# Kernel optimization log

Hardware: AMD Instinct MI355X
Metric: run time of the kernel (lower is better)

The kernel has to match this reference:

```python
import jax, jax.numpy as jnp
import numpy as np

EMBED = 1024
HEADS = 16
HEAD_DIM = EMBED // HEADS


def setup_inputs() -> dict:
    key = jax.random.key(0)
    ks = jax.random.split(key, 8)
    N, L = 2, 2048
    values = jax.random.normal(ks[0], (N, L, EMBED), dtype=jnp.float32)
    keys_ = jax.random.normal(ks[1], (N, L, EMBED), dtype=jnp.float32)
    query = jax.random.normal(ks[2], (N, L, EMBED), dtype=jnp.float32)
    mask = jnp.ones((N, 1, 1, L), dtype=jnp.int32)
    s = 1.0 / np.sqrt(EMBED)
    W_q = jax.random.normal(ks[3], (EMBED, EMBED), dtype=jnp.float32) * s
    W_k = jax.random.normal(ks[4], (EMBED, EMBED), dtype=jnp.float32) * s
    W_v = jax.random.normal(ks[5], (EMBED, EMBED), dtype=jnp.float32) * s
    W_o = jax.random.normal(ks[6], (EMBED, EMBED), dtype=jnp.float32) * s
    b_o = jax.random.normal(ks[7], (EMBED,), dtype=jnp.float32) * 0.01
    return {"values": values, "keys": keys_, "query": query, "mask": mask,
            "W_q": W_q, "W_k": W_k, "W_v": W_v, "W_o": W_o, "b_o": b_o}


def reference(values, keys, query, mask, W_q, W_k, W_v, W_o, b_o):
    N, Lq, _ = query.shape
    Lk = keys.shape[1]
    # projections (torch Linear: x @ W.T); reshape to (N, H, L, Dh)
    q = (query @ W_q.T).reshape(N, Lq, HEADS, HEAD_DIM).transpose(0, 2, 1, 3)
    k = (keys @ W_k.T).reshape(N, Lk, HEADS, HEAD_DIM).transpose(0, 2, 1, 3)
    v = (values @ W_v.T).reshape(N, Lk, HEADS, HEAD_DIM).transpose(0, 2, 1, 3)
    energy = jnp.einsum('bhqd,bhkd->bhqk', q, k) / jnp.sqrt(jnp.float32(HEAD_DIM))
    energy = jnp.where(mask == 0, jnp.float32(-1e20), energy)
    attn = jax.nn.softmax(energy, axis=-1)
    out = jnp.einsum('bhqk,bhkd->bhqd', attn, v)
    out = out.transpose(0, 2, 1, 3).reshape(N, Lq, EMBED)
    return out @ W_o.T + b_o
```

## Files before the change

### kernel.cpp

```cpp
#include <hip/hip_runtime.h>
#include <cstddef>
#include <cstdint>

#define SEQ    2048
#define NBATCH 2

typedef unsigned short u16;
typedef unsigned int   u32;
typedef __attribute__((ext_vector_type(8))) short bf16x8;
typedef __attribute__((ext_vector_type(4))) float f32x4;

#if __has_builtin(__builtin_amdgcn_exp2f)
#define EXP2F(x) __builtin_amdgcn_exp2f(x)
#else
#define EXP2F(x) exp2f(x)
#endif

__device__ __forceinline__ u32 fbits(float x) { union { float f; u32 u; } c; c.f = x; return c.u; }
__device__ __forceinline__ u16 f2bf(float x) { return (u16)((fbits(x) + 0x8000u) >> 16); }
__device__ __forceinline__ u32 pack2bf(float lo, float hi) {
    return __builtin_amdgcn_perm(fbits(hi) + 0x8000u, fbits(lo) + 0x8000u, 0x07060302u);
}

__global__ __launch_bounds__(256)
void cast3(const float* __restrict__ a, const float* __restrict__ b, const float* __restrict__ c,
           u16* __restrict__ oa, u16* __restrict__ ob, u16* __restrict__ oc, int n4)
{
    const float* s; u16* d;
    if (blockIdx.y == 0)      { s = a; d = oa; }
    else if (blockIdx.y == 1) { s = b; d = ob; }
    else                      { s = c; d = oc; }
    int i = blockIdx.x * 256 + threadIdx.x;
    if (i >= n4) return;
    float4 v = ((const float4*)s)[i];
    uint2 r; r.x = pack2bf(v.x, v.y); r.y = pack2bf(v.z, v.w);
    ((uint2*)d)[i] = r;
}

__global__ __launch_bounds__(256)
void cast4(const float* __restrict__ a, const float* __restrict__ b,
           const float* __restrict__ c, const float* __restrict__ e,
           u16* __restrict__ oa, u16* __restrict__ ob, u16* __restrict__ oc, u16* __restrict__ oe,
           int n4)
{
    const float* s; u16* d;
    if (blockIdx.y == 0)      { s = a; d = oa; }
    else if (blockIdx.y == 1) { s = b; d = ob; }
    else if (blockIdx.y == 2) { s = c; d = oc; }
    else                      { s = e; d = oe; }
    int i = blockIdx.x * 256 + threadIdx.x;
    if (i >= n4) return;
    float4 v = ((const float4*)s)[i];
    uint2 r; r.x = pack2bf(v.x, v.y); r.y = pack2bf(v.z, v.w);
    ((uint2*)d)[i] = r;
}

__device__ __forceinline__
void gemm_body(const u16* __restrict__ X, const u16* __restrict__ W,
               void* __restrict__ Yv, const float* __restrict__ bias, const int layout,
               const int kbeg, const int kend)
{
    __shared__ u16 smem[2 * 128 * 72];
    u16* As = smem;
    u16* Bs = smem + 128 * 72;

    const int tid  = threadIdx.x;
    const int wave = tid >> 6;
    const int lane = tid & 63;
    const int lm   = lane & 15;
    const int quad = lane >> 4;
    const int m0 = blockIdx.x * 128;
    const int n0 = blockIdx.y * 128;
    const int wr = (wave & 1) * 64;
    const int wc = (wave >> 1) * 64;

    const int srow = tid >> 1;
    const int scol = (tid & 1) * 32;
    const u16* xg = X + (size_t)(m0 + srow) * 1024 + scol;
    const u16* wg = W + (size_t)(n0 + srow) * 1024 + scol;

    bf16x8 pa[4], pb[4];
    #pragma unroll
    for (int p = 0; p < 4; ++p) {
        pa[p] = *(const bf16x8*)(xg + kbeg + p * 8);
        pb[p] = *(const bf16x8*)(wg + kbeg + p * 8);
    }

    f32x4 acc[4][4] = {};

    for (int k0 = kbeg; k0 < kend; k0 += 64) {
        __syncthreads();
        #pragma unroll
        for (int p = 0; p < 4; ++p) {
            *(bf16x8*)&As[srow * 72 + scol + p * 8] = pa[p];
            *(bf16x8*)&Bs[srow * 72 + scol + p * 8] = pb[p];
        }
        __syncthreads();
        if (k0 + 64 < kend) {
            #pragma unroll
            for (int p = 0; p < 4; ++p) {
                pa[p] = *(const bf16x8*)(xg + k0 + 64 + p * 8);
                pb[p] = *(const bf16x8*)(wg + k0 + 64 + p * 8);
            }
        }
        #pragma unroll
        for (int kk = 0; kk < 64; kk += 32) {
            bf16x8 af[4], bf[4];
            #pragma unroll
            for (int t = 0; t < 4; ++t) {
                af[t] = *(const bf16x8*)&As[(wr + t * 16 + lm) * 72 + kk + quad * 8];
                bf[t] = *(const bf16x8*)&Bs[(wc + t * 16 + lm) * 72 + kk + quad * 8];
            }
            #pragma unroll
            for (int i = 0; i < 4; ++i)
                #pragma unroll
                for (int j = 0; j < 4; ++j)
                    acc[i][j] = __builtin_amdgcn_mfma_f32_16x16x32_bf16(af[i], bf[j], acc[i][j], 0, 0, 0);
        }
    }

    if (layout == 3) {
        float* Y = (float*)Yv;
        #pragma unroll
        for (int i = 0; i < 4; ++i)
            #pragma unroll
            for (int j = 0; j < 4; ++j) {
                const int C = n0 + wc + j * 16 + lm;
                const float bv = bias ? bias[C] : 0.0f;
                #pragma unroll
                for (int r = 0; r < 4; ++r) {
                    const int R = m0 + wr + i * 16 + quad * 4 + r;
                    Y[(size_t)R * 1024 + C] = acc[i][j][r] + bv;
                }
            }
    } else if (layout == 0) {
        u16* Y = (u16*)Yv;
        #pragma unroll
        for (int i = 0; i < 4; ++i)
            #pragma unroll
            for (int j = 0; j < 4; ++j) {
                const int C = n0 + wc + j * 16 + lm;
                #pragma unroll
                for (int r = 0; r < 4; ++r) {
                    const int R = m0 + wr + i * 16 + quad * 4 + r;
                    Y[(size_t)R * 1024 + C] = f2bf(acc[i][j][r]);
                }
            }
    } else {
        __syncthreads();
        u16* T = smem;
        #pragma unroll
        for (int i = 0; i < 4; ++i)
            #pragma unroll
            for (int j = 0; j < 4; ++j) {
                const int col = wc + j * 16 + lm;
                const int row = wr + i * 16 + quad * 4;
                uint2 v;
                v.x = pack2bf(acc[i][j][0], acc[i][j][1]);
                v.y = pack2bf(acc[i][j][2], acc[i][j][3]);
                *(uint2*)&T[col * 132 + row] = v;
            }
        __syncthreads();
        const int dp = tid >> 1, half = (tid & 1) * 64;
        const int nn = m0 >> 11, l0 = m0 & 2047;
        const int C = n0 + dp, h = C >> 6, d = C & 63;
        u16* Y = (u16*)Yv;
        const size_t base = (((size_t)nn * 16 + h) * 64 + d) * SEQ + l0 + half;
        #pragma unroll
        for (int p = 0; p < 8; ++p) {
            bf16x8 v = *(const bf16x8*)&T[dp * 132 + half + p * 8];
            *(bf16x8*)(Y + base + p * 8) = v;
        }
    }
}

__global__ __launch_bounds__(256, 2)
void gemm_qkv(const u16* __restrict__ xq, const u16* __restrict__ xk, const u16* __restrict__ xv,
              const u16* __restrict__ wq, const u16* __restrict__ wk, const u16* __restrict__ wv,
              u16* __restrict__ qb, u16* __restrict__ kb, u16* __restrict__ vt)
{
    if (blockIdx.z == 0)      gemm_body(xq, wq, qb, nullptr, 0, 0, 1024);
    else if (blockIdx.z == 1) gemm_body(xk, wk, kb, nullptr, 0, 0, 1024);
    else                      gemm_body(xv, wv, vt, nullptr, 2, 0, 1024);
}

__global__ __launch_bounds__(256, 2)
void gemm_out_split(const u16* __restrict__ X, const u16* __restrict__ W,
                    float* __restrict__ p0, float* __restrict__ p1)
{
    if (blockIdx.z == 0) gemm_body(X, W, p0, nullptr, 3, 0, 512);
    else                 gemm_body(X, W, p1, nullptr, 3, 512, 1024);
}

__global__ __launch_bounds__(256)
void reduce_bias(const float* __restrict__ p0, const float* __restrict__ p1,
                 const float* __restrict__ bias, float* __restrict__ out)
{
    const int i = blockIdx.x * 256 + threadIdx.x;
    float4 a = ((const float4*)p0)[i];
    float4 b = ((const float4*)p1)[i];
    float4 c = ((const float4*)bias)[i & 255];
    float4 o;
    o.x = a.x + b.x + c.x; o.y = a.y + b.y + c.y;
    o.z = a.z + b.z + c.z; o.w = a.w + b.w + c.w;
    ((float4*)out)[i] = o;
}

__global__ __launch_bounds__(256, 2)
void flash_attn_bf16(const u16* __restrict__ Qb, const u16* __restrict__ Kb,
                     const u16* __restrict__ VT, const int* __restrict__ mask,
                     u16* __restrict__ O)
{
    __shared__ u16 Ks[128 * 72];
    __shared__ u16 Vts[64 * 136];
    __shared__ u16 Ps[4][32 * 72];

    const int tid  = threadIdx.x;
    const int wave = tid >> 6;
    const int lane = tid & 63;
    const int lm   = lane & 15;
    const int quad = lane >> 4;
    const int h = blockIdx.y, n = blockIdx.z;
    const int wq = blockIdx.x * 128 + wave * 32;

    const u16* Qh = Qb + ((size_t)n * SEQ) * 1024 + h * 64;
    const u16* Kh = Kb + ((size_t)n * SEQ) * 1024 + h * 64;
    const u16* Vh = VT + (((size_t)n * 16 + h) * 64) * SEQ;
    const int* mk = mask + (size_t)n * SEQ;
    u16* Pw = &Ps[wave][0];

    bf16x8 qf[2][2];
    #pragma unroll
    for (int t = 0; t < 2; ++t)
        #pragma unroll
        for (int s = 0; s < 2; ++s)
            qf[t][s] = *(const bf16x8*)(Qh + (size_t)(wq + t * 16 + lm) * 1024 + s * 32 + quad * 8);

    f32x4 o_acc[2][4] = {};
    float l_i[2][4] = {};

    const int kr = tid >> 1, kc = (tid & 1) * 32;
    const int vr = tid >> 2, vc = (tid & 3) * 32;

    bf16x8 ka[4], va[4];
    #pragma unroll
    for (int p = 0; p < 4; ++p) {
        ka[p] = *(const bf16x8*)(Kh + (size_t)kr * 1024 + kc + p * 8);
        va[p] = *(const bf16x8*)(Vh + (size_t)vr * SEQ + vc + p * 8);
    }

    const float cs = 0.125f * 1.44269504f;

    for (int c0 = 0; c0 < SEQ; c0 += 128) {
        __syncthreads();
        #pragma unroll
        for (int p = 0; p < 4; ++p) {
            *(bf16x8*)&Ks[kr * 72 + kc + p * 8]   = ka[p];
            *(bf16x8*)&Vts[vr * 136 + vc + p * 8] = va[p];
        }
        __syncthreads();

        if (c0 + 128 < SEQ) {
            #pragma unroll
            for (int p = 0; p < 4; ++p) {
                ka[p] = *(const bf16x8*)(Kh + (size_t)(c0 + 128 + kr) * 1024 + kc + p * 8);
                va[p] = *(const bf16x8*)(Vh + (size_t)vr * SEQ + c0 + 128 + vc + p * 8);
            }
        }

        f32x4 s[2][8] = {};
        #pragma unroll
        for (int nt = 0; nt < 8; ++nt) {
            bf16x8 kf0 = *(const bf16x8*)&Ks[(nt * 16 + lm) * 72 + quad * 8];
            bf16x8 kf1 = *(const bf16x8*)&Ks[(nt * 16 + lm) * 72 + 32 + quad * 8];
            #pragma unroll
            for (int t = 0; t < 2; ++t) {
                s[t][nt] = __builtin_amdgcn_mfma_f32_16x16x32_bf16(qf[t][0], kf0, s[t][nt], 0, 0, 0);
                s[t][nt] = __builtin_amdgcn_mfma_f32_16x16x32_bf16(qf[t][1], kf1, s[t][nt], 0, 0, 0);
            }
        }

        int msk[8];
        #pragma unroll
        for (int nt = 0; nt < 8; ++nt) msk[nt] = mk[c0 + nt * 16 + lm];
        #pragma unroll
        for (int t = 0; t < 2; ++t)
            #pragma unroll
            for (int nt = 0; nt < 8; ++nt)
                #pragma unroll
                for (int r = 0; r < 4; ++r) {
                    float e = EXP2F(s[t][nt][r] * cs);
                    e = msk[nt] ? e : 0.0f;
                    s[t][nt][r] = e;
                    l_i[t][r] += e;
                }

        #pragma unroll
        for (int half = 0; half < 2; ++half) {
            #pragma unroll
            for (int t = 0; t < 2; ++t)
                #pragma unroll
                for (int ntl = 0; ntl < 4; ++ntl)
                    #pragma unroll
                    for (int r = 0; r < 4; ++r)
                        Pw[(t * 16 + quad * 4 + r) * 72 + ntl * 16 + lm] =
                            f2bf(s[t][half * 4 + ntl][r]);

            #pragma unroll
            for (int ksl = 0; ksl < 2; ++ksl) {
                bf16x8 pf[2];
                #pragma unroll
                for (int t = 0; t < 2; ++t)
                    pf[t] = *(const bf16x8*)&Pw[(t * 16 + lm) * 72 + ksl * 32 + quad * 8];
                #pragma unroll
                for (int dt = 0; dt < 4; ++dt) {
                    bf16x8 vf = *(const bf16x8*)&Vts[(dt * 16 + lm) * 136 + half * 64 + ksl * 32 + quad * 8];
                    #pragma unroll
                    for (int t = 0; t < 2; ++t)
                        o_acc[t][dt] = __builtin_amdgcn_mfma_f32_16x16x32_bf16(pf[t], vf, o_acc[t][dt], 0, 0, 0);
                }
            }
        }
    }

    #pragma unroll
    for (int t = 0; t < 2; ++t)
        #pragma unroll
        for (int r = 0; r < 4; ++r) {
            float v = l_i[t][r];
            #pragma unroll
            for (int off = 1; off < 16; off <<= 1) v += __shfl_xor(v, off);
            l_i[t][r] = 1.0f / v;
        }
    #pragma unroll
    for (int t = 0; t < 2; ++t)
        #pragma unroll
        for (int dt = 0; dt < 4; ++dt)
            #pragma unroll
            for (int r = 0; r < 4; ++r) {
                const int ql = wq + t * 16 + quad * 4 + r;
                const int col = h * 64 + dt * 16 + lm;
                O[((size_t)n * SEQ + ql) * 1024 + col] = f2bf(o_acc[t][dt][r] * l_i[t][r]);
            }
}

extern "C" void kernel_launch(void* const* d_in, const int* in_sizes, int n_in,
                              void* d_out, int out_size, void* d_ws, size_t ws_size,
                              hipStream_t stream)
{
    const float* values = (const float*)d_in[0];
    const float* keys   = (const float*)d_in[1];
    const float* query  = (const float*)d_in[2];
    const int*   mask   = (const int*)d_in[3];
    const float* W_q    = (const float*)d_in[4];
    const float* W_k    = (const float*)d_in[5];
    const float* W_v    = (const float*)d_in[6];
    const float* W_o    = (const float*)d_in[7];
    const float* b_o    = (const float*)d_in[8];

    const size_t NTOK = (size_t)NBATCH * SEQ * 1024;
    const size_t WSZ  = 1024 * 1024;
    u16* p = (u16*)d_ws;
    u16* qb    = p; p += NTOK;
    u16* kb    = p; p += NTOK;
    u16* vt    = p; p += NTOK;
    u16* xq    = p; p += NTOK;
    u16* xk    = p; p += NTOK;
    u16* xv    = p; p += NTOK;
    u16* attnb = p; p += NTOK;
    u16* wqb   = p; p += WSZ;
    u16* wkb   = p; p += WSZ;
    u16* wvb   = p; p += WSZ;
    u16* wob   = p; p += WSZ;
    float* part0 = (float*)qb;
    float* part1 = (float*)vt;

    cast3<<<dim3(4096, 3), 256, 0, stream>>>(query, keys, values, xq, xk, xv, (int)(NTOK / 4));
    cast4<<<dim3(1024, 4), 256, 0, stream>>>(W_q, W_k, W_v, W_o, wqb, wkb, wvb, wob, (int)(WSZ / 4));

    gemm_qkv<<<dim3(32, 8, 3), 256, 0, stream>>>(xq, xk, xv, wqb, wkb, wvb, qb, kb, vt);

    flash_attn_bf16<<<dim3(16, 16, 2), 256, 0, stream>>>(qb, kb, vt, mask, attnb);

    gemm_out_split<<<dim3(32, 8, 2), 256, 0, stream>>>(attnb, wob, part0, part1);
    reduce_bias<<<4096, 256, 0, stream>>>(part0, part1, b_o, (float*)d_out);
}
```

Before: 236.9 us.

## Keep attention probabilities in registers and replace split-K output GEMM with 64-wide tiles

The attention kernel now computes S transposed (K as the A operand) so that each lane's exp values map directly onto the operand layout of the 16x16x16 bf16 MFMA. This removes the per-wave LDS staging buffer for P and its store and reload round-trip, and it also removes that LDS allocation. Row sums are reduced with fewer shuffles, and the mask is loaded as int4 vectors. The output projection drops split-K plus the separate reduce kernel and uses a 128x64 tile with the bias fused into the epilogue. This avoids the fp32 partial buffer round-trip and one launch, at the cost of a smaller-K MFMA instruction in the PV product.

```diff
diff --git a/kernel.cpp b/kernel.cpp
--- a/kernel.cpp
+++ b/kernel.cpp
@@ -8,6 +8,7 @@
 typedef unsigned short u16;
 typedef unsigned int   u32;
 typedef __attribute__((ext_vector_type(8))) short bf16x8;
+typedef __attribute__((ext_vector_type(4))) short bf16x4;
 typedef __attribute__((ext_vector_type(4))) float f32x4;
 
 #if __has_builtin(__builtin_amdgcn_exp2f)
@@ -16,10 +17,15 @@
 #define EXP2F(x) exp2f(x)
 #endif
 
+#define MFMA_K16(a, b, c) __builtin_amdgcn_mfma_f32_16x16x16bf16_1k(a, b, c, 0, 0, 0)
+
 __device__ __forceinline__ u32 fbits(float x) { union { float f; u32 u; } c; c.f = x; return c.u; }
 __device__ __forceinline__ u16 f2bf(float x) { return (u16)((fbits(x) + 0x8000u) >> 16); }
 __device__ __forceinline__ u32 pack2bf(float lo, float hi) {
     return __builtin_amdgcn_perm(fbits(hi) + 0x8000u, fbits(lo) + 0x8000u, 0x07060302u);
+}
+__device__ __forceinline__ bf16x4 mk_bf16x4(u32 lo, u32 hi) {
+    union { u32 w[2]; bf16x4 v; } u; u.w[0] = lo; u.w[1] = hi; return u.v;
 }
 
 __global__ __launch_bounds__(256)
@@ -57,8 +63,7 @@
 
 __device__ __forceinline__
 void gemm_body(const u16* __restrict__ X, const u16* __restrict__ W,
-               void* __restrict__ Yv, const float* __restrict__ bias, const int layout,
-               const int kbeg, const int kend)
+               void* __restrict__ Yv, const int layout)
 {
     __shared__ u16 smem[2 * 128 * 72];
     u16* As = smem;
@@ -82,13 +87,13 @@
     bf16x8 pa[4], pb[4];
     #pragma unroll
     for (int p = 0; p < 4; ++p) {
-        pa[p] = *(const bf16x8*)(xg + kbeg + p * 8);
-        pb[p] = *(const bf16x8*)(wg + kbeg + p * 8);
+        pa[p] = *(const bf16x8*)(xg + p * 8);
+        pb[p] = *(const bf16x8*)(wg + p * 8);
     }
 
     f32x4 acc[4][4] = {};
 
-    for (int k0 = kbeg; k0 < kend; k0 += 64) {
+    for (int k0 = 0; k0 < 1024; k0 += 64) {
         __syncthreads();
         #pragma unroll
         for (int p = 0; p < 4; ++p) {
@@ -96,7 +101,7 @@
             *(bf16x8*)&Bs[srow * 72 + scol + p * 8] = pb[p];
         }
         __syncthreads();
-        if (k0 + 64 < kend) {
+        if (k0 + 64 < 1024) {
             #pragma unroll
             for (int p = 0; p < 4; ++p) {
                 pa[p] = *(const bf16x8*)(xg + k0 + 64 + p * 8);
@@ -119,21 +124,7 @@
         }
     }
 
-    if (layout == 3) {
-        float* Y = (float*)Yv;
-        #pragma unroll
-        for (int i = 0; i < 4; ++i)
-            #pragma unroll
-            for (int j = 0; j < 4; ++j) {
-                const int C = n0 + wc + j * 16 + lm;
-                const float bv = bias ? bias[C] : 0.0f;
-                #pragma unroll
-                for (int r = 0; r < 4; ++r) {
-                    const int R = m0 + wr + i * 16 + quad * 4 + r;
-                    Y[(size_t)R * 1024 + C] = acc[i][j][r] + bv;
-                }
-            }
-    } else if (layout == 0) {
+    if (layout == 0) {
         u16* Y = (u16*)Yv;
         #pragma unroll
         for (int i = 0; i < 4; ++i)
@@ -179,31 +170,83 @@
               const u16* __restrict__ wq, const u16* __restrict__ wk, const u16* __restrict__ wv,
               u16* __restrict__ qb, u16* __restrict__ kb, u16* __restrict__ vt)
 {
-    if (blockIdx.z == 0)      gemm_body(xq, wq, qb, nullptr, 0, 0, 1024);
-    else if (blockIdx.z == 1) gemm_body(xk, wk, kb, nullptr, 0, 0, 1024);
-    else                      gemm_body(xv, wv, vt, nullptr, 2, 0, 1024);
+    if (blockIdx.z == 0)      gemm_body(xq, wq, qb, 0);
+    else if (blockIdx.z == 1) gemm_body(xk, wk, kb, 0);
+    else                      gemm_body(xv, wv, vt, 2);
 }
 
 __global__ __launch_bounds__(256, 2)
-void gemm_out_split(const u16* __restrict__ X, const u16* __restrict__ W,
-                    float* __restrict__ p0, float* __restrict__ p1)
-{
-    if (blockIdx.z == 0) gemm_body(X, W, p0, nullptr, 3, 0, 512);
-    else                 gemm_body(X, W, p1, nullptr, 3, 512, 1024);
-}
-
-__global__ __launch_bounds__(256)
-void reduce_bias(const float* __restrict__ p0, const float* __restrict__ p1,
-                 const float* __restrict__ bias, float* __restrict__ out)
-{
-    const int i = blockIdx.x * 256 + threadIdx.x;
-    float4 a = ((const float4*)p0)[i];
-    float4 b = ((const float4*)p1)[i];
-    float4 c = ((const float4*)bias)[i & 255];
-    float4 o;
-    o.x = a.x + b.x + c.x; o.y = a.y + b.y + c.y;
-    o.z = a.z + b.z + c.z; o.w = a.w + b.w + c.w;
-    ((float4*)out)[i] = o;
+void gemm_out64(const u16* __restrict__ X, const u16* __restrict__ W,
+                float* __restrict__ Y, const float* __restrict__ bias)
+{
+    __shared__ u16 As[128 * 72];
+    __shared__ u16 Bs[64 * 72];
+
+    const int tid  = threadIdx.x;
+    const int wave = tid >> 6;
+    const int lane = tid & 63;
+    const int lm   = lane & 15;
+    const int quad = lane >> 4;
+    const int m0 = blockIdx.x * 128;
+    const int n0 = blockIdx.y * 64;
+    const int wr = (wave & 1) * 64;
+    const int wc = (wave >> 1) * 32;
+
+    const int arow = tid >> 1, acol = (tid & 1) * 32;
+    const int brow = tid >> 2, bcol = (tid & 3) * 16;
+    const u16* xg = X + (size_t)(m0 + arow) * 1024 + acol;
+    const u16* wg = W + (size_t)(n0 + brow) * 1024 + bcol;
+
+    bf16x8 pa[4], pb[2];
+    #pragma unroll
+    for (int p = 0; p < 4; ++p) pa[p] = *(const bf16x8*)(xg + p * 8);
+    #pragma unroll
+    for (int p = 0; p < 2; ++p) pb[p] = *(const bf16x8*)(wg + p * 8);
+
+    f32x4 acc[4][2] = {};
+
+    for (int k0 = 0; k0 < 1024; k0 += 64) {
+        __syncthreads();
+        #pragma unroll
+        for (int p = 0; p < 4; ++p) *(bf16x8*)&As[arow * 72 + acol + p * 8] = pa[p];
+        #pragma unroll
+        for (int p = 0; p < 2; ++p) *(bf16x8*)&Bs[brow * 72 + bcol + p * 8] = pb[p];
+        __syncthreads();
+        if (k0 + 64 < 1024) {
+            #pragma unroll
+            for (int p = 0; p < 4; ++p) pa[p] = *(const bf16x8*)(xg + k0 + 64 + p * 8);
+            #pragma unroll
+            for (int p = 0; p < 2; ++p) pb[p] = *(const bf16x8*)(wg + k0 + 64 + p * 8);
+        }
+        #pragma unroll
+        for (int kk = 0; kk < 64; kk += 32) {
+            bf16x8 af[4], bf[2];
+            #pragma unroll
+            for (int t = 0; t < 4; ++t)
+                af[t] = *(const bf16x8*)&As[(wr + t * 16 + lm) * 72 + kk + quad * 8];
+            #pragma unroll
+            for (int j = 0; j < 2; ++j)
+                bf[j] = *(const bf16x8*)&Bs[(wc + j * 16 + lm) * 72 + kk + quad * 8];
+            #pragma unroll
+            for (int i = 0; i < 4; ++i)
+                #pragma unroll
+                for (int j = 0; j < 2; ++j)
+                    acc[i][j] = __builtin_amdgcn_mfma_f32_16x16x32_bf16(af[i], bf[j], acc[i][j], 0, 0, 0);
+        }
+    }
+
+    #pragma unroll
+    for (int i = 0; i < 4; ++i)
+        #pragma unroll
+        for (int j = 0; j < 2; ++j) {
+            const int C = n0 + wc + j * 16 + lm;
+            const float bv = bias[C];
+            #pragma unroll
+            for (int r = 0; r < 4; ++r) {
+                const int R = m0 + wr + i * 16 + quad * 4 + r;
+                Y[(size_t)R * 1024 + C] = acc[i][j][r] + bv;
+            }
+        }
 }
 
 __global__ __launch_bounds__(256, 2)
@@ -213,7 +256,6 @@
 {
     __shared__ u16 Ks[128 * 72];
     __shared__ u16 Vts[64 * 136];
-    __shared__ u16 Ps[4][32 * 72];
 
     const int tid  = threadIdx.x;
     const int wave = tid >> 6;
@@ -227,17 +269,16 @@
     const u16* Kh = Kb + ((size_t)n * SEQ) * 1024 + h * 64;
     const u16* Vh = VT + (((size_t)n * 16 + h) * 64) * SEQ;
     const int* mk = mask + (size_t)n * SEQ;
-    u16* Pw = &Ps[wave][0];
 
     bf16x8 qf[2][2];
     #pragma unroll
-    for (int t = 0; t < 2; ++t)
-        #pragma unroll
-        for (int s = 0; s < 2; ++s)
-            qf[t][s] = *(const bf16x8*)(Qh + (size_t)(wq + t * 16 + lm) * 1024 + s * 32 + quad * 8);
+    for (int qt = 0; qt < 2; ++qt)
+        #pragma unroll
+        for (int ks = 0; ks < 2; ++ks)
+            qf[qt][ks] = *(const bf16x8*)(Qh + (size_t)(wq + qt * 16 + lm) * 1024 + ks * 32 + quad * 8);
 
     f32x4 o_acc[2][4] = {};
-    float l_i[2][4] = {};
+    float l_i[2] = {};
 
     const int kr = tid >> 1, kc = (tid & 1) * 32;
     const int vr = tid >> 2, vc = (tid & 3) * 32;
@@ -268,79 +309,72 @@
             }
         }
 
-        f32x4 s[2][8] = {};
-        #pragma unroll
-        for (int nt = 0; nt < 8; ++nt) {
-            bf16x8 kf0 = *(const bf16x8*)&Ks[(nt * 16 + lm) * 72 + quad * 8];
-            bf16x8 kf1 = *(const bf16x8*)&Ks[(nt * 16 + lm) * 72 + 32 + quad * 8];
-            #pragma unroll
-            for (int t = 0; t < 2; ++t) {
-                s[t][nt] = __builtin_amdgcn_mfma_f32_16x16x32_bf16(qf[t][0], kf0, s[t][nt], 0, 0, 0);
-                s[t][nt] = __builtin_amdgcn_mfma_f32_16x16x32_bf16(qf[t][1], kf1, s[t][nt], 0, 0, 0);
-            }
-        }
-
-        int msk[8];
-        #pragma unroll
-        for (int nt = 0; nt < 8; ++nt) msk[nt] = mk[c0 + nt * 16 + lm];
-        #pragma unroll
-        for (int t = 0; t < 2; ++t)
-            #pragma unroll
-            for (int nt = 0; nt < 8; ++nt)
+        int4 mkv[8];
+        #pragma unroll
+        for (int kt = 0; kt < 8; ++kt)
+            mkv[kt] = *(const int4*)(mk + c0 + kt * 16 + quad * 4);
+
+        f32x4 st[8][2] = {};
+        #pragma unroll
+        for (int kt = 0; kt < 8; ++kt) {
+            bf16x8 kf0 = *(const bf16x8*)&Ks[(kt * 16 + lm) * 72 + quad * 8];
+            bf16x8 kf1 = *(const bf16x8*)&Ks[(kt * 16 + lm) * 72 + 32 + quad * 8];
+            #pragma unroll
+            for (int qt = 0; qt < 2; ++qt) {
+                st[kt][qt] = __builtin_amdgcn_mfma_f32_16x16x32_bf16(kf0, qf[qt][0], st[kt][qt], 0, 0, 0);
+                st[kt][qt] = __builtin_amdgcn_mfma_f32_16x16x32_bf16(kf1, qf[qt][1], st[kt][qt], 0, 0, 0);
+            }
+        }
+
+        bf16x4 pf[8][2];
+        #pragma unroll
+        for (int kt = 0; kt < 8; ++kt) {
+            const int4 mv = mkv[kt];
+            const int mm[4] = {mv.x, mv.y, mv.z, mv.w};
+            #pragma unroll
+            for (int qt = 0; qt < 2; ++qt) {
+                float e[4];
                 #pragma unroll
                 for (int r = 0; r < 4; ++r) {
-                    float e = EXP2F(s[t][nt][r] * cs);
-                    e = msk[nt] ? e : 0.0f;
-                    s[t][nt][r] = e;
-                    l_i[t][r] += e;
+                    float v = EXP2F(st[kt][qt][r] * cs);
+                    v = mm[r] ? v : 0.0f;
+                    e[r] = v;
+                    l_i[qt] += v;
                 }
-
-        #pragma unroll
-        for (int half = 0; half < 2; ++half) {
-            #pragma unroll
-            for (int t = 0; t < 2; ++t)
+                pf[kt][qt] = mk_bf16x4(pack2bf(e[0], e[1]), pack2bf(e[2], e[3]));
+            }
+        }
+
+        #pragma unroll
+        for (int kt = 0; kt < 8; ++kt)
+            #pragma unroll
+            for (int dt = 0; dt < 4; ++dt) {
+                bf16x4 vf = *(const bf16x4*)&Vts[(dt * 16 + lm) * 136 + kt * 16 + quad * 4];
                 #pragma unroll
-                for (int ntl = 0; ntl < 4; ++ntl)
-                    #pragma unroll
-                    for (int r = 0; r < 4; ++r)
-                        Pw[(t * 16 + quad * 4 + r) * 72 + ntl * 16 + lm] =
-                            f2bf(s[t][half * 4 + ntl][r]);
-
-            #pragma unroll
-            for (int ksl = 0; ksl < 2; ++ksl) {
-                bf16x8 pf[2];
-                #pragma unroll
-                for (int t = 0; t < 2; ++t)
-                    pf[t] = *(const bf16x8*)&Pw[(t * 16 + lm) * 72 + ksl * 32 + quad * 8];
-                #pragma unroll
-                for (int dt = 0; dt < 4; ++dt) {
-                    bf16x8 vf = *(const bf16x8*)&Vts[(dt * 16 + lm) * 136 + half * 64 + ksl * 32 + quad * 8];
-                    #pragma unroll
-                    for (int t = 0; t < 2; ++t)
-                        o_acc[t][dt] = __builtin_amdgcn_mfma_f32_16x16x32_bf16(pf[t], vf, o_acc[t][dt], 0, 0, 0);
-                }
-            }
-        }
-    }
-
-    #pragma unroll
-    for (int t = 0; t < 2; ++t)
-        #pragma unroll
-        for (int r = 0; r < 4; ++r) {
-            float v = l_i[t][r];
-            #pragma unroll
-            for (int off = 1; off < 16; off <<= 1) v += __shfl_xor(v, off);
-            l_i[t][r] = 1.0f / v;
-        }
-    #pragma unroll
-    for (int t = 0; t < 2; ++t)
+                for (int qt = 0; qt < 2; ++qt)
+                    o_acc[qt][dt] = MFMA_K16(pf[kt][qt], vf, o_acc[qt][dt]);
+            }
+    }
+
+    float linv[2][4];
+    #pragma unroll
+    for (int qt = 0; qt < 2; ++qt) {
+        float v = l_i[qt];
+        v += __shfl_xor(v, 16);
+        v += __shfl_xor(v, 32);
+        #pragma unroll
+        for (int r = 0; r < 4; ++r)
+            linv[qt][r] = 1.0f / __shfl(v, quad * 4 + r);
+    }
+    #pragma unroll
+    for (int qt = 0; qt < 2; ++qt)
         #pragma unroll
         for (int dt = 0; dt < 4; ++dt)
             #pragma unroll
             for (int r = 0; r < 4; ++r) {
-                const int ql = wq + t * 16 + quad * 4 + r;
+                const int ql = wq + qt * 16 + quad * 4 + r;
                 const int col = h * 64 + dt * 16 + lm;
-                O[((size_t)n * SEQ + ql) * 1024 + col] = f2bf(o_acc[t][dt][r] * l_i[t][r]);
+                O[((size_t)n * SEQ + ql) * 1024 + col] = f2bf(o_acc[qt][dt][r] * linv[qt][r]);
             }
 }
 
@@ -372,8 +406,6 @@
     u16* wkb   = p; p += WSZ;
     u16* wvb   = p; p += WSZ;
     u16* wob   = p; p += WSZ;
-    float* part0 = (float*)qb;
-    float* part1 = (float*)vt;
 
     cast3<<<dim3(4096, 3), 256, 0, stream>>>(query, keys, values, xq, xk, xv, (int)(NTOK / 4));
     cast4<<<dim3(1024, 4), 256, 0, stream>>>(W_q, W_k, W_v, W_o, wqb, wkb, wvb, wob, (int)(WSZ / 4));
@@ -382,6 +414,5 @@
 
     flash_attn_bf16<<<dim3(16, 16, 2), 256, 0, stream>>>(qb, kb, vt, mask, attnb);
 
-    gemm_out_split<<<dim3(32, 8, 2), 256, 0, stream>>>(attnb, wob, part0, part1);
-    reduce_bias<<<4096, 256, 0, stream>>>(part0, part1, b_o, (float*)d_out);
-}
+    gemm_out64<<<dim3(32, 16), 256, 0, stream>>>(attnb, wob, (float*)d_out, b_o);
+}
```

Result: no change. 237.1 us (+0.1%).
